# Kernel optimization log

Measured on AMD Instinct MI355X. Metric: run time of the kernel, lower is better.

Reference implementation:

```python
import jax, jax.numpy as jnp
import numpy as np
from jax import lax

# Fixed LBP neighbor-difference filters: each of 8 filters is (neighbor - center)
_LBP_W = np.array([
    [[[0,0,1],[0,-1,0],[0,0,0]]],
    [[[0,0,0],[0,-1,1],[0,0,0]]],
    [[[0,0,0],[0,-1,0],[0,0,1]]],
    [[[0,0,0],[0,-1,0],[0,1,0]]],
    [[[0,0,0],[0,-1,0],[1,0,0]]],
    [[[0,0,0],[1,-1,0],[0,0,0]]],
    [[[1,0,0],[0,-1,0],[0,0,0]]],
    [[[0,1,0],[0,-1,0],[0,0,0]]],
], dtype=np.float32)  # [8,1,3,3] OIHW

_RGB2GRAY = np.array([0.299, 0.587, 0.114], dtype=np.float32)


def setup_inputs() -> dict:
    key = jax.random.key(0)
    img = jax.random.uniform(key, (16, 3, 1024, 1024), dtype=jnp.float32)
    lbp_weight = jnp.asarray(_LBP_W)                                   # [8,1,3,3]
    kernel_weight = jnp.asarray(2.0 ** np.arange(8, dtype=np.float32)  # 1,2,...,128
                                ).reshape(1, 8, 1, 1)
    return {"img": img, "lbp_weight": lbp_weight, "kernel_weight": kernel_weight}


def reference(img, lbp_weight, kernel_weight):
    # rgb2gray: [B,3,H,W] -> [B,1,H,W]
    gray = jnp.einsum("bchw,c->bhw", img, jnp.asarray(_RGB2GRAY))[:, None]
    # 3x3 LBP neighbor-difference conv, padding=1 (SAME)
    out = lax.conv_general_dilated(
        gray, lbp_weight, window_strides=(1, 1), padding=((1, 1), (1, 1)),
        dimension_numbers=("NCHW", "OIHW", "NCHW"))                    # [B,8,H,W]
    # threshold then weighted sum of bit-planes -> LBP code in [0,255]
    bits = jnp.where(out >= 0.0, 1.0, 0.0)
    lbp_img = jnp.sum(bits * kernel_weight, axis=1)                     # [B,H,W]
    # 256-bin histogram over ALL elements (matches torch.where counting loop)
    idx = lbp_img.astype(jnp.int32).reshape(-1)
    hist = jnp.zeros((1, 256), dtype=jnp.float32).at[0, idx].add(1.0)
    # standardize with unbiased std (torch.std default, ddof=1)
    mean = jnp.mean(hist, axis=1, keepdims=True)
    std = jnp.sqrt(jnp.sum((hist - mean) ** 2, axis=1, keepdims=True) / (256 - 1))
    return (hist - mean) / std
```

## Files before the change

kernel.cpp:

```cpp
#include <hip/hip_runtime.h>

#define TX 64
#define TY 32
#define TILE_H 34
#define TILE_W 72
#define NTX (1024 / TX)
#define NTY (1024 / TY)
#define NBATCH 16
#define NTILES (NTX * NTY * NBATCH)
#define NBLOCKS 2048
#define NHIST 8

__global__ void lbp_zero_hist(unsigned* __restrict__ g_hist) {
    g_hist[blockIdx.x * 256 + threadIdx.x] = 0u;
}

__global__ __launch_bounds__(256) void lbp_hist_kernel(
        const float* __restrict__ img, unsigned* __restrict__ g_hist) {
    __shared__ __align__(16) float tile[TILE_H][TILE_W];
    __shared__ unsigned s_hist[4][256];
    const int tid = threadIdx.x;
    const int wv  = tid >> 6;
    #pragma unroll
    for (int w = 0; w < 4; ++w) s_hist[w][tid] = 0u;

    const int tx = tid & 63;
    const int ry = wv * 8;

    for (int t = blockIdx.x; t < NTILES; t += NBLOCKS) {
        const int bx  = t % NTX;
        const int rem = t / NTX;
        const int by  = rem % NTY;
        const int b   = rem / NTY;
        const int y0  = by * TY - 1;
        const int xq0 = bx * TX - 4;
        const float* imgb = img + (size_t)b * 3u * 1024u * 1024u;

        __syncthreads();

        for (int it = tid; it < TILE_H * 18; it += 256) {
            const int row = it / 18;
            const int q   = it - row * 18;
            const int gy  = y0 + row;
            const int gxq = xq0 + (q << 2);
            float4 gv = make_float4(0.f, 0.f, 0.f, 0.f);
            if ((unsigned)gy < 1024u) {
                const float* rowp = imgb + (size_t)gy * 1024u;
                if ((unsigned)gxq <= 1020u) {
                    const float4 r4 = *(const float4*)(rowp + gxq);
                    const float4 g4 = *(const float4*)(rowp + 1048576u + gxq);
                    const float4 b4 = *(const float4*)(rowp + 2097152u + gxq);
                    gv.x = (r4.x * 0.299f + g4.x * 0.587f) + b4.x * 0.114f;
                    gv.y = (r4.y * 0.299f + g4.y * 0.587f) + b4.y * 0.114f;
                    gv.z = (r4.z * 0.299f + g4.z * 0.587f) + b4.z * 0.114f;
                    gv.w = (r4.w * 0.299f + g4.w * 0.587f) + b4.w * 0.114f;
                } else {
                    #pragma unroll
                    for (int k = 0; k < 4; ++k) {
                        const int gx = gxq + k;
                        if ((unsigned)gx < 1024u) {
                            const float r  = rowp[gx];
                            const float g  = rowp[1048576u + gx];
                            const float bb = rowp[2097152u + gx];
                            ((float*)&gv)[k] = (r * 0.299f + g * 0.587f) + bb * 0.114f;
                        }
                    }
                }
            }
            *(float4*)&tile[row][q << 2] = gv;
        }
        __syncthreads();

        float c00 = tile[ry    ][tx + 3], c01 = tile[ry    ][tx + 4], c02 = tile[ry    ][tx + 5];
        float c10 = tile[ry + 1][tx + 3], c11 = tile[ry + 1][tx + 4], c12 = tile[ry + 1][tx + 5];
        #pragma unroll
        for (int p = 0; p < 8; ++p) {
            const float c20 = tile[ry + p + 2][tx + 3];
            const float c21 = tile[ry + p + 2][tx + 4];
            const float c22 = tile[ry + p + 2][tx + 5];
            const unsigned code =
                (c02 >= c11 ? 1u   : 0u) |
                (c12 >= c11 ? 2u   : 0u) |
                (c22 >= c11 ? 4u   : 0u) |
                (c21 >= c11 ? 8u   : 0u) |
                (c20 >= c11 ? 16u  : 0u) |
                (c10 >= c11 ? 32u  : 0u) |
                (c00 >= c11 ? 64u  : 0u) |
                (c01 >= c11 ? 128u : 0u);
            atomicAdd(&s_hist[wv][code], 1u);
            c00 = c10; c01 = c11; c02 = c12;
            c10 = c20; c11 = c21; c12 = c22;
        }
    }

    __syncthreads();
    const unsigned total = s_hist[0][tid] + s_hist[1][tid] + s_hist[2][tid] + s_hist[3][tid];
    atomicAdd(&g_hist[((blockIdx.x & (NHIST - 1)) << 8) + tid], total);
}

__global__ __launch_bounds__(256) void lbp_finalize(
        const unsigned* __restrict__ g_hist, float* __restrict__ out) {
    __shared__ float red[256];
    const int i = threadIdx.x;
    unsigned hv = 0u;
    #pragma unroll
    for (int c = 0; c < NHIST; ++c) hv += g_hist[(c << 8) + i];
    const float h = (float)hv;
    red[i] = h;
    __syncthreads();
    #pragma unroll
    for (int s = 128; s > 0; s >>= 1) {
        if (i < s) red[i] += red[i + s];
        __syncthreads();
    }
    const float mean = red[0] * (1.0f / 256.0f);
    __syncthreads();
    const float d = h - mean;
    red[i] = d * d;
    __syncthreads();
    #pragma unroll
    for (int s = 128; s > 0; s >>= 1) {
        if (i < s) red[i] += red[i + s];
        __syncthreads();
    }
    const float stdv = sqrtf(red[0] * (1.0f / 255.0f));
    out[i] = d / stdv;
}

extern "C" void kernel_launch(void* const* d_in, const int* in_sizes, int n_in,
                              void* d_out, int out_size, void* d_ws, size_t ws_size,
                              hipStream_t stream) {
    const float* img = (const float*)d_in[0];
    unsigned* g_hist = (unsigned*)d_ws;
    float* out = (float*)d_out;

    lbp_zero_hist<<<NHIST, 256, 0, stream>>>(g_hist);
    lbp_hist_kernel<<<NBLOCKS, 256, 0, stream>>>(img, g_hist);
    lbp_finalize<<<1, 256, 0, stream>>>(g_hist, out);
}
```

Baseline: 284.5 us.

## Enlarge tiles and compute four LBP pixels per thread with float4 LDS reads

Tiles grow from 64x32 to 128x64 pixels, and the block count is halved. Each thread now computes a 4-wide by 8-tall strip, reading neighbours as float4 from shared memory. The goal is fewer LDS loads per pixel, a smaller halo overhead and cheaper tile index math using shifts. The cost is more registers and larger shared memory per block, which could reduce occupancy, and four shared atomics back to back per row.

Measured after the change: 287.0 us. Within noise of the previous version (+0.9%).

```diff
diff --git a/kernel.cpp b/kernel.cpp
--- a/kernel.cpp
+++ b/kernel.cpp
@@ -1,14 +1,15 @@
 #include <hip/hip_runtime.h>
 
-#define TX 64
-#define TY 32
-#define TILE_H 34
-#define TILE_W 72
+#define TX 128
+#define TY 64
+#define TILE_H 66
+#define TILE_W 136
+#define QROW 34
 #define NTX (1024 / TX)
 #define NTY (1024 / TY)
 #define NBATCH 16
 #define NTILES (NTX * NTY * NBATCH)
-#define NBLOCKS 2048
+#define NBLOCKS 1024
 #define NHIST 8
 
 __global__ void lbp_zero_hist(unsigned* __restrict__ g_hist) {
@@ -24,23 +25,25 @@
     #pragma unroll
     for (int w = 0; w < 4; ++w) s_hist[w][tid] = 0u;
 
-    const int tx = tid & 63;
-    const int ry = wv * 8;
+    const int g  = tid & 31;
+    const int s  = tid >> 5;
+    const int cg = g << 2;
+    const int r0 = s << 3;
 
     for (int t = blockIdx.x; t < NTILES; t += NBLOCKS) {
-        const int bx  = t % NTX;
-        const int rem = t / NTX;
-        const int by  = rem % NTY;
-        const int b   = rem / NTY;
+        const int bx  = t & (NTX - 1);
+        const int rem = t >> 3;
+        const int by  = rem & (NTY - 1);
+        const int b   = rem >> 4;
         const int y0  = by * TY - 1;
         const int xq0 = bx * TX - 4;
         const float* imgb = img + (size_t)b * 3u * 1024u * 1024u;
 
         __syncthreads();
 
-        for (int it = tid; it < TILE_H * 18; it += 256) {
-            const int row = it / 18;
-            const int q   = it - row * 18;
+        for (int it = tid; it < TILE_H * QROW; it += 256) {
+            const int row = it / QROW;
+            const int q   = it - row * QROW;
             const int gy  = y0 + row;
             const int gxq = xq0 + (q << 2);
             float4 gv = make_float4(0.f, 0.f, 0.f, 0.f);
@@ -60,9 +63,9 @@
                         const int gx = gxq + k;
                         if ((unsigned)gx < 1024u) {
                             const float r  = rowp[gx];
-                            const float g  = rowp[1048576u + gx];
+                            const float gc = rowp[1048576u + gx];
                             const float bb = rowp[2097152u + gx];
-                            ((float*)&gv)[k] = (r * 0.299f + g * 0.587f) + bb * 0.114f;
+                            ((float*)&gv)[k] = (r * 0.299f + gc * 0.587f) + bb * 0.114f;
                         }
                     }
                 }
@@ -71,25 +74,44 @@
         }
         __syncthreads();
 
-        float c00 = tile[ry    ][tx + 3], c01 = tile[ry    ][tx + 4], c02 = tile[ry    ][tx + 5];
-        float c10 = tile[ry + 1][tx + 3], c11 = tile[ry + 1][tx + 4], c12 = tile[ry + 1][tx + 5];
+        float  al = tile[r0    ][cg + 3];
+        float4 am = *(const float4*)&tile[r0    ][cg + 4];
+        float  ar = tile[r0    ][cg + 8];
+        float  bl = tile[r0 + 1][cg + 3];
+        float4 bm = *(const float4*)&tile[r0 + 1][cg + 4];
+        float  br = tile[r0 + 1][cg + 8];
         #pragma unroll
         for (int p = 0; p < 8; ++p) {
-            const float c20 = tile[ry + p + 2][tx + 3];
-            const float c21 = tile[ry + p + 2][tx + 4];
-            const float c22 = tile[ry + p + 2][tx + 5];
-            const unsigned code =
-                (c02 >= c11 ? 1u   : 0u) |
-                (c12 >= c11 ? 2u   : 0u) |
-                (c22 >= c11 ? 4u   : 0u) |
-                (c21 >= c11 ? 8u   : 0u) |
-                (c20 >= c11 ? 16u  : 0u) |
-                (c10 >= c11 ? 32u  : 0u) |
-                (c00 >= c11 ? 64u  : 0u) |
-                (c01 >= c11 ? 128u : 0u);
-            atomicAdd(&s_hist[wv][code], 1u);
-            c00 = c10; c01 = c11; c02 = c12;
-            c10 = c20; c11 = c21; c12 = c22;
+            const int rb = r0 + p + 2;
+            const float  cl2 = tile[rb][cg + 3];
+            const float4 cm  = *(const float4*)&tile[rb][cg + 4];
+            const float  cr2 = tile[rb][cg + 8];
+            const float c0 = bm.x;
+            const unsigned code0 =
+                (am.y >= c0 ? 1u:0u) | (bm.y >= c0 ? 2u:0u) | (cm.y >= c0 ? 4u:0u) |
+                (cm.x >= c0 ? 8u:0u) | (cl2  >= c0 ? 16u:0u) | (bl  >= c0 ? 32u:0u) |
+                (al   >= c0 ? 64u:0u) | (am.x >= c0 ? 128u:0u);
+            const float c1 = bm.y;
+            const unsigned code1 =
+                (am.z >= c1 ? 1u:0u) | (bm.z >= c1 ? 2u:0u) | (cm.z >= c1 ? 4u:0u) |
+                (cm.y >= c1 ? 8u:0u) | (cm.x >= c1 ? 16u:0u) | (bm.x >= c1 ? 32u:0u) |
+                (am.x >= c1 ? 64u:0u) | (am.y >= c1 ? 128u:0u);
+            const float c2 = bm.z;
+            const unsigned code2 =
+                (am.w >= c2 ? 1u:0u) | (bm.w >= c2 ? 2u:0u) | (cm.w >= c2 ? 4u:0u) |
+                (cm.z >= c2 ? 8u:0u) | (cm.y >= c2 ? 16u:0u) | (bm.y >= c2 ? 32u:0u) |
+                (am.y >= c2 ? 64u:0u) | (am.z >= c2 ? 128u:0u);
+            const float c3 = bm.w;
+            const unsigned code3 =
+                (ar   >= c3 ? 1u:0u) | (br   >= c3 ? 2u:0u) | (cr2  >= c3 ? 4u:0u) |
+                (cm.w >= c3 ? 8u:0u) | (cm.z >= c3 ? 16u:0u) | (bm.z >= c3 ? 32u:0u) |
+                (am.z >= c3 ? 64u:0u) | (am.w >= c3 ? 128u:0u);
+            atomicAdd(&s_hist[wv][code0], 1u);
+            atomicAdd(&s_hist[wv][code1], 1u);
+            atomicAdd(&s_hist[wv][code2], 1u);
+            atomicAdd(&s_hist[wv][code3], 1u);
+            al = bl; am = bm; ar = br;
+            bl = cl2; bm = cm; br = cr2;
         }
     }
 
```
